# Optimization experiments

Measured on AMD Instinct MI355X. Metric: run time of the kernel, lower is better.

## Reference

```python
import jax, jax.numpy as jnp
import numpy as np

N, E, D, T, R, H = 100000, 800000, 128, 4, 4, 8
DK = D // H
LN_EPS = 1e-5


def _per_type_proj(x, W, b, node_type):
    # x:[N,D], W:[T,D,D], b:[T,D] -> select projection by each node's type
    proj = jnp.einsum('ni,tio->nto', x, W) + b[None]          # [N,T,D]
    return jnp.take_along_axis(proj, node_type[:, None, None], axis=1)[:, 0]  # [N,D]


def setup_inputs() -> dict:
    key = jax.random.key(0)
    ks = jax.random.split(key, 12)
    sW = 1.0 / np.sqrt(D)
    sR = np.sqrt(2.0 / (DK + DK))  # glorot for [dk,dk]
    return {
        'x': jax.random.normal(ks[0], (N, D), jnp.float32),
        'node_type': jax.random.randint(ks[1], (N,), 0, T, jnp.int32),
        'edge_index': jax.random.randint(ks[2], (2, E), 0, N, jnp.int32),
        'edge_type': jax.random.randint(ks[3], (E,), 0, R, jnp.int32),
        'edge_spatial': jnp.zeros((E,), jnp.int32),
        'Wk': jax.random.normal(ks[4], (T, D, D), jnp.float32) * sW,
        'bk': jnp.zeros((T, D), jnp.float32),
        'Wq': jax.random.normal(ks[5], (T, D, D), jnp.float32) * sW,
        'bq': jnp.zeros((T, D), jnp.float32),
        'Wv': jax.random.normal(ks[6], (T, D, D), jnp.float32) * sW,
        'bv': jnp.zeros((T, D), jnp.float32),
        'Wa': jax.random.normal(ks[7], (T, D, D), jnp.float32) * sW,
        'ba': jnp.zeros((T, D), jnp.float32),
        'rel_pri': jnp.ones((R, H), jnp.float32),
        'rel_att': jax.random.normal(ks[8], (R, H, DK, DK), jnp.float32) * sR,
        'rel_msg': jax.random.normal(ks[9], (R, H, DK, DK), jnp.float32) * sR,
        'skip': jnp.ones((T,), jnp.float32),
        'ln_gamma': jnp.ones((T, D), jnp.float32),
        'ln_beta': jnp.zeros((T, D), jnp.float32),
    }


def reference(x, node_type, edge_index, edge_type, edge_spatial,
              Wk, bk, Wq, bq, Wv, bv, Wa, ba,
              rel_pri, rel_att, rel_msg, skip, ln_gamma, ln_beta):
    src, dst = edge_index[0], edge_index[1]  # PyG: row0 = source j, row1 = target i

    # per-type linear projections, selected by node type
    K = _per_type_proj(x, Wk, bk, node_type)
    Q = _per_type_proj(x, Wq, bq, node_type)
    V = _per_type_proj(x, Wv, bv, node_type)

    q_e = Q[dst].reshape(E, H, DK)
    k_e = K[src].reshape(E, H, DK)
    v_e = V[src].reshape(E, H, DK)

    # per-relation transforms without materializing [E,H,DK,DK] gathers
    k_rel = jnp.zeros_like(k_e)
    msg = jnp.zeros_like(v_e)
    for r in range(R):
        m = (edge_type == r)[:, None, None]
        k_rel = k_rel + jnp.where(m, jnp.einsum('ehd,hdk->ehk', k_e, rel_att[r]), 0.0)
        msg = msg + jnp.where(m, jnp.einsum('ehd,hdk->ehk', v_e, rel_msg[r]), 0.0)

    logits = (q_e * k_rel).sum(-1) * rel_pri[edge_type] / np.sqrt(DK)  # [E,H]

    # segment softmax over destination nodes
    seg_max = jax.ops.segment_max(logits, dst, num_segments=N)
    seg_max = jnp.where(jnp.isfinite(seg_max), seg_max, 0.0)
    ex = jnp.exp(logits - seg_max[dst])
    denom = jax.ops.segment_sum(ex, dst, num_segments=N)
    att = ex / denom[dst]  # [E,H]

    aggr = jax.ops.segment_sum(msg * att[:, :, None], dst, num_segments=N)  # [N,H,DK]
    h = jax.nn.gelu(aggr.reshape(N, D), approximate=False)

    trans = _per_type_proj(h, Wa, ba, node_type)
    alpha = jax.nn.sigmoid(skip)[node_type][:, None]
    pre = trans * alpha + x * (1.0 - alpha)

    # per-type LayerNorm
    mu = pre.mean(-1, keepdims=True)
    var = ((pre - mu) ** 2).mean(-1, keepdims=True)
    norm = (pre - mu) * jax.lax.rsqrt(var + LN_EPS)
    return norm * ln_gamma[node_type] + ln_beta[node_type]
```

## Files before the change

kernel.cpp:

```cpp
#include <hip/hip_runtime.h>
#include <math.h>

#define D_DIM 128

using bf16x8 = __attribute__((ext_vector_type(8))) short;
using f32x4  = __attribute__((ext_vector_type(4))) float;

__device__ __forceinline__ unsigned short f2bf(float f) {
    unsigned u = __float_as_uint(f);
    u += 0x7fffu + ((u >> 16) & 1u);
    return (unsigned short)(u >> 16);
}

__global__ __launch_bounds__(256)
void count_types_k(const int* __restrict__ nt, int* __restrict__ blockcnt, int N) {
    __shared__ int wcnt[4][4];
    int tid = threadIdx.x;
    int i = blockIdx.x * 256 + tid;
    int w = tid >> 6, l = tid & 63;
    int t = (i < N) ? nt[i] : -1;
    #pragma unroll
    for (int tt = 0; tt < 4; ++tt) {
        unsigned long long m = __ballot(t == tt);
        if (l == 0) wcnt[w][tt] = __popcll(m);
    }
    __syncthreads();
    if (tid < 4) {
        blockcnt[blockIdx.x * 4 + tid] =
            wcnt[0][tid] + wcnt[1][tid] + wcnt[2][tid] + wcnt[3][tid];
    }
}

__global__ __launch_bounds__(256)
void scan_blocks_k(const int* __restrict__ blockcnt, int nb, int N,
                   int* __restrict__ boff, int* __restrict__ pad_off,
                   int* __restrict__ order_p) {
    __shared__ int tot_s[4];
    __shared__ int po_s[5];
    int tid = threadIdx.x;
    int t = tid >> 6, l = tid & 63;
    int sum = 0;
    for (int base = 0; base < nb; base += 64) {
        int b = base + l;
        sum += (b < nb) ? blockcnt[b * 4 + t] : 0;
    }
    #pragma unroll
    for (int m = 1; m < 64; m <<= 1) sum += __shfl_xor(sum, m);
    if (l == 0) tot_s[t] = sum;
    __syncthreads();
    if (tid == 0) {
        int s = 0;
        for (int tt = 0; tt < 4; ++tt) { po_s[tt] = s; s += ((tot_s[tt] + 63) >> 6) << 6; }
        po_s[4] = s;
        for (int tt = 0; tt < 5; ++tt) pad_off[tt] = po_s[tt];
    }
    __syncthreads();
    #pragma unroll 1
    for (int tt = 0; tt < 4; ++tt) {
        int gs = po_s[tt] + tot_s[tt], ge = po_s[tt + 1];
        for (int i = gs + tid; i < ge; i += 256) order_p[i] = -1;
    }
    for (int i = po_s[4] + tid; i < N + 320; i += 256) order_p[i] = -1;
    __syncthreads();
    int run = po_s[t];
    for (int base = 0; base < nb; base += 64) {
        int b = base + l;
        int v = (b < nb) ? blockcnt[b * 4 + t] : 0;
        int incl = v;
        #pragma unroll
        for (int off = 1; off < 64; off <<= 1) {
            int up = __shfl_up(incl, off);
            if (l >= off) incl += up;
        }
        if (b < nb) boff[b * 4 + t] = run + incl - v;
        run += __shfl(incl, 63);
    }
}

__global__ __launch_bounds__(256)
void scatter_types_k(const int* __restrict__ nt, const int* __restrict__ boff,
                     int* __restrict__ order_p, int N) {
    __shared__ int wbase[4][4];
    int tid = threadIdx.x;
    int i = blockIdx.x * 256 + tid;
    int w = tid >> 6, l = tid & 63;
    int t = (i < N) ? nt[i] : -1;
    int rank = 0;
    #pragma unroll
    for (int tt = 0; tt < 4; ++tt) {
        unsigned long long m = __ballot(t == tt);
        if (l == 0) wbase[w][tt] = __popcll(m);
        if (t == tt) rank = __popcll(m & ((1ull << l) - 1ull));
    }
    __syncthreads();
    if (tid < 4) {
        int run = 0;
        for (int ww = 0; ww < 4; ++ww) { int c = wbase[ww][tid]; wbase[ww][tid] = run; run += c; }
    }
    __syncthreads();
    if (i < N) order_p[boff[blockIdx.x * 4 + t] + wbase[w][t] + rank] = i;
}

__global__ __launch_bounds__(256)
void prep_weights_k(const float* __restrict__ Wk, const float* __restrict__ Wq,
                    const float* __restrict__ Wv, const float* __restrict__ Wa,
                    const float* __restrict__ bk, const float* __restrict__ bv,
                    const float* __restrict__ rel_att, const float* __restrict__ rel_msg,
                    const float* __restrict__ rel_pri,
                    unsigned short* __restrict__ Wqt, unsigned short* __restrict__ Wat,
                    unsigned short* __restrict__ Wkrt, unsigned short* __restrict__ Wvmt,
                    float* __restrict__ bkr, float* __restrict__ bvm) {
    int idx = blockIdx.x * 256 + threadIdx.x;
    int i = idx & 127;
    int col = (idx >> 7) & 127;
    int r = (idx >> 14) & 3;
    int t = idx >> 16;
    int h = col >> 4, k = col & 15;
    {
        const float* wk = Wk + t * 16384 + i * 128 + h * 16;
        const float* wv = Wv + t * 16384 + i * 128 + h * 16;
        const float* ra = rel_att + ((r * 8 + h) * 16) * 16 + k;
        const float* rm = rel_msg + ((r * 8 + h) * 16) * 16 + k;
        float s1 = 0.f, s2 = 0.f;
        #pragma unroll
        for (int d = 0; d < 16; ++d) {
            s1 += wk[d] * ra[d * 16];
            s2 += wv[d] * rm[d * 16];
        }
        Wkrt[idx] = f2bf(s1 * rel_pri[r * 8 + h] * 0.25f);
        Wvmt[idx] = f2bf(s2);
    }
    if (idx < 65536) {
        int t2 = idx >> 14, rem = idx & 16383, row = rem >> 7, col2 = rem & 127;
        int d = (t2 << 14) | (col2 << 7) | row;
        Wqt[d] = f2bf(Wq[idx]);
        Wat[d] = f2bf(Wa[idx]);
    }
    if (idx < 4096) {
        int bi = idx & 2047;
        int col3 = bi & 127, r3 = (bi >> 7) & 3, t3 = bi >> 9;
        int h3 = col3 >> 4, k3 = col3 & 15;
        float s = 0.f;
        if (idx < 2048) {
            #pragma unroll
            for (int d = 0; d < 16; ++d)
                s += bk[t3 * 128 + h3 * 16 + d] * rel_att[((r3 * 8 + h3) * 16 + d) * 16 + k3];
            bkr[bi] = s * rel_pri[r3 * 8 + h3] * 0.25f;
        } else {
            #pragma unroll
            for (int d = 0; d < 16; ++d)
                s += bv[t3 * 128 + h3 * 16 + d] * rel_msg[((r3 * 8 + h3) * 16 + d) * 16 + k3];
            bvm[bi] = s;
        }
    }
}

__global__ void deg_k(const int* __restrict__ ei, int* __restrict__ deg, int E) {
    int e = blockIdx.x * 256 + threadIdx.x;
    if (e < E) atomicAdd(&deg[ei[E + e]], 1);
}
__global__ void scan1_k(const int* __restrict__ deg, int* __restrict__ excl,
                        int* __restrict__ bsum, int N) {
    __shared__ int s[512];
    int i = blockIdx.x * 512 + threadIdx.x;
    int v = (i < N) ? deg[i] : 0;
    s[threadIdx.x] = v;
    __syncthreads();
    for (int off = 1; off < 512; off <<= 1) {
        int t = (threadIdx.x >= off) ? s[threadIdx.x - off] : 0;
        __syncthreads();
        s[threadIdx.x] += t;
        __syncthreads();
    }
    if (i < N) excl[i] = s[threadIdx.x] - v;
    if (threadIdx.x == 511) bsum[blockIdx.x] = s[511];
}
__global__ void scan2_k(int* __restrict__ bsum, int nb) {
    int l = threadIdx.x & 63;
    int run = 0;
    for (int base = 0; base < nb; base += 64) {
        int b = base + l;
        int v = (b < nb) ? bsum[b] : 0;
        int incl = v;
        #pragma unroll
        for (int off = 1; off < 64; off <<= 1) {
            int up = __shfl_up(incl, off);
            if (l >= off) incl += up;
        }
        if (b < nb) bsum[b] = run + incl - v;
        run += __shfl(incl, 63);
    }
}
__global__ void scan3_k(int* __restrict__ excl, const int* __restrict__ bsum, int N) {
    int i = blockIdx.x * 512 + threadIdx.x;
    if (i < N) excl[i] += bsum[blockIdx.x];
}
__global__ void scatter_edges_k(const int* __restrict__ ei, const int* __restrict__ et,
                                const int* __restrict__ off, int* __restrict__ cursor,
                                int* __restrict__ elist, int E) {
    int e = blockIdx.x * 256 + threadIdx.x;
    if (e < E) {
        int dst = ei[E + e];
        int p = off[dst] + atomicAdd(&cursor[dst], 1);
        elist[p] = (ei[e] << 2) | et[e];
    }
}

__global__ __launch_bounds__(256, 4)
void proj_mfma(const float* __restrict__ x, const int* __restrict__ order_p,
               const int* __restrict__ pad_off,
               const unsigned short* __restrict__ Wqt, const float* __restrict__ bq,
               const unsigned short* __restrict__ W_kr_t, const float* __restrict__ bkr,
               const unsigned short* __restrict__ W_vm_t, const float* __restrict__ bvm,
               unsigned short* __restrict__ Qb, unsigned short* __restrict__ KRb,
               unsigned short* __restrict__ VMb, int N) {
    __shared__ unsigned shmem[64 * 128];
    __shared__ int gid_s[64];
    unsigned* xs = shmem;
    char* stageb = (char*)shmem;
    int tid = threadIdx.x;
    int base = blockIdx.x * 64;
    int t = (base >= pad_off[1]) + (base >= pad_off[2]) + (base >= pad_off[3]);

    if (tid < 64) gid_s[tid] = order_p[base + tid];
    __syncthreads();

    {
        int row = tid >> 2, q = tid & 3;
        int g = gid_s[row];
        const float4* xr = (const float4*)(x + (size_t)(g < 0 ? 0 : g) * 128 + q * 32);
        int swz = (row & 7) << 4;
        #pragma unroll
        for (int v4 = 0; v4 < 8; ++v4) {
            float4 f = (g >= 0) ? xr[v4] : make_float4(0.f, 0.f, 0.f, 0.f);
            unsigned ua = (unsigned)f2bf(f.x) | ((unsigned)f2bf(f.y) << 16);
            unsigned ub = (unsigned)f2bf(f.z) | ((unsigned)f2bf(f.w) << 16);
            int c2 = (q * 16 + v4 * 2) * 4;
            xs[(row << 6) + (((c2) ^ swz) >> 2)] = ua;
            xs[(row << 6) + (((c2 + 4) ^ swz) >> 2)] = ub;
        }
    }
    __syncthreads();

    int w = tid >> 6, l = tid & 63;
    int lr = l & 15, lg = l >> 4;

    bf16x8 afr[4][4];
    #pragma unroll
    for (int j = 0; j < 4; ++j) {
        int row = j * 16 + lr;
        #pragma unroll
        for (int ks = 0; ks < 4; ++ks) {
            int byteoff = (ks * 64 + lg * 16) ^ ((lr & 7) << 4);
            afr[j][ks] = *reinterpret_cast<const bf16x8*>(
                reinterpret_cast<const char*>(&xs[row << 6]) + byteoff);
        }
    }
    __syncthreads();

    #pragma unroll 1
    for (int pass = 0; pass < 4; ++pass) {
        int m0 = (pass & 1) * 2;
        const unsigned short* Wp;
        const float* bp;
        unsigned short* dstp;
        if (pass < 2) { Wp = W_kr_t; bp = bkr; dstp = KRb; }
        else          { Wp = W_vm_t; bp = bvm; dstp = VMb; }
        Wp += (size_t)(t * 4 + m0) << 14;
        bp += (t * 4 + m0) * 128;

        #pragma unroll
        for (int ci = 0; ci < 2; ++ci) {
            int c = w * 2 + ci;
            #pragma unroll
            for (int mm = 0; mm < 2; ++mm) {
                const unsigned short* wb = Wp + ((size_t)mm << 14)
                                         + (size_t)(c * 16 + lr) * 128 + lg * 8;
                bf16x8 wfr[4];
                #pragma unroll
                for (int ks = 0; ks < 4; ++ks) wfr[ks] = *(const bf16x8*)(wb + ks * 32);
                f32x4 acc0 = {0.f,0.f,0.f,0.f}, acc1 = {0.f,0.f,0.f,0.f};
                f32x4 acc2 = {0.f,0.f,0.f,0.f}, acc3 = {0.f,0.f,0.f,0.f};
                #pragma unroll
                for (int ks = 0; ks < 4; ++ks) {
                    acc0 = __builtin_amdgcn_mfma_f32_16x16x32_bf16(wfr[ks], afr[0][ks], acc0, 0, 0, 0);
                    acc1 = __builtin_amdgcn_mfma_f32_16x16x32_bf16(wfr[ks], afr[1][ks], acc1, 0, 0, 0);
                    acc2 = __builtin_amdgcn_mfma_f32_16x16x32_bf16(wfr[ks], afr[2][ks], acc2, 0, 0, 0);
                    acc3 = __builtin_amdgcn_mfma_f32_16x16x32_bf16(wfr[ks], afr[3][ks], acc3, 0, 0, 0);
                }
                float4 bb = *(const float4*)&bp[mm * 128 + c * 16 + lg * 4];
                int colb = (mm * 128 + c * 16 + lg * 4) * 2;
                f32x4 accs[4] = {acc0, acc1, acc2, acc3};
                #pragma unroll
                for (int j = 0; j < 4; ++j) {
                    int node = j * 16 + lr;
                    unsigned p0 = (unsigned)f2bf(accs[j][0] + bb.x) | ((unsigned)f2bf(accs[j][1] + bb.y) << 16);
                    unsigned p1 = (unsigned)f2bf(accs[j][2] + bb.z) | ((unsigned)f2bf(accs[j][3] + bb.w) << 16);
                    int byte = (node * 512 + colb) ^ ((node & 7) << 4);
                    *(uint2*)(stageb + byte) = make_uint2(p0, p1);
                }
            }
        }
        __syncthreads();
        #pragma unroll
        for (int i = 0; i < 8; ++i) {
            int row = w * 16 + i * 2 + (l >> 5);
            int l32 = l & 31;
            int byte = (row * 512 + l32 * 16) ^ ((row & 7) << 4);
            uint4 v = *(const uint4*)(stageb + byte);
            int g = gid_s[row];
            if (g >= 0)
                *(uint4*)&dstp[(size_t)g * 512 + (pass & 1) * 256 + l32 * 8] = v;
        }
        __syncthreads();
    }

    #pragma unroll
    for (int ci = 0; ci < 2; ++ci) {
        int c = w * 2 + ci;
        const unsigned short* wb = Wqt + ((size_t)t << 14) + (size_t)(c * 16 + lr) * 128 + lg * 8;
        bf16x8 wfr[4];
        #pragma unroll
        for (int ks = 0; ks < 4; ++ks) wfr[ks] = *(const bf16x8*)(wb + ks * 32);
        f32x4 acc0 = {0.f,0.f,0.f,0.f}, acc1 = {0.f,0.f,0.f,0.f};
        f32x4 acc2 = {0.f,0.f,0.f,0.f}, acc3 = {0.f,0.f,0.f,0.f};
        #pragma unroll
        for (int ks = 0; ks < 4; ++ks) {
            acc0 = __builtin_amdgcn_mfma_f32_16x16x32_bf16(wfr[ks], afr[0][ks], acc0, 0, 0, 0);
            acc1 = __builtin_amdgcn_mfma_f32_16x16x32_bf16(wfr[ks], afr[1][ks], acc1, 0, 0, 0);
            acc2 = __builtin_amdgcn_mfma_f32_16x16x32_bf16(wfr[ks], afr[2][ks], acc2, 0, 0, 0);
            acc3 = __builtin_amdgcn_mfma_f32_16x16x32_bf16(wfr[ks], afr[3][ks], acc3, 0, 0, 0);
        }
        float4 bb = *(const float4*)&bq[t * 128 + c * 16 + lg * 4];
        int colb = (c * 16 + lg * 4) * 2;
        f32x4 accs[4] = {acc0, acc1, acc2, acc3};
        #pragma unroll
        for (int j = 0; j < 4; ++j) {
            int node = j * 16 + lr;
            unsigned p0 = (unsigned)f2bf(accs[j][0] + bb.x) | ((unsigned)f2bf(accs[j][1] + bb.y) << 16);
            unsigned p1 = (unsigned)f2bf(accs[j][2] + bb.z) | ((unsigned)f2bf(accs[j][3] + bb.w) << 16);
            int byte = (node * 256 + colb) ^ ((node & 7) << 4);
            *(uint2*)(stageb + byte) = make_uint2(p0, p1);
        }
    }
    __syncthreads();
    #pragma unroll
    for (int i = 0; i < 4; ++i) {
        int row = w * 16 + i * 4 + (l >> 4);
        int l16 = l & 15;
        int byte = (row * 256 + l16 * 16) ^ ((row & 7) << 4);
        uint4 v = *(const uint4*)(stageb + byte);
        int g = gid_s[row];
        if (g >= 0) *(uint4*)&Qb[(size_t)g * 128 + l16 * 8] = v;
    }
}

__global__ __launch_bounds__(256)
void edge_fused(const unsigned short* __restrict__ Qb,
                const unsigned short* __restrict__ KRb,
                const unsigned short* __restrict__ VMb,
                const int* __restrict__ off, const int* __restrict__ elist,
                float* __restrict__ aggr, int N, int E) {
    int w = threadIdx.x >> 6, l = threadIdx.x & 63;
    int dstA = (blockIdx.x * 4 + w) * 2;
    if (dstA >= N) return;
    int dstB = dstA + 1;
    bool hasB = (dstB < N);
    int q = l >> 4, c = l & 15;

    float QfA[8], QfB[8];
    {
        bf16x8 qv = *(const bf16x8*)&Qb[(size_t)dstA * 128 + c * 8];
        const unsigned* qu = (const unsigned*)&qv;
        #pragma unroll
        for (int i = 0; i < 4; ++i) {
            QfA[2*i]   = __uint_as_float(qu[i] << 16);
            QfA[2*i+1] = __uint_as_float(qu[i] & 0xffff0000u);
        }
    }
    {
        bf16x8 qv = *(const bf16x8*)&Qb[(size_t)(hasB ? dstB : dstA) * 128 + c * 8];
        const unsigned* qu = (const unsigned*)&qv;
        #pragma unroll
        for (int i = 0; i < 4; ++i) {
            QfB[2*i]   = __uint_as_float(qu[i] << 16);
            QfB[2*i+1] = __uint_as_float(qu[i] & 0xffff0000u);
        }
    }

    int eA0 = off[dstA];
    int eA1 = hasB ? off[dstB] : E;
    int eB0 = eA1;
    int eB1 = hasB ? ((dstB == N - 1) ? E : off[dstB + 1]) : eA1;
    int degA = eA1 - eA0;
    int degB = eB1 - eB0;
    int mdeg = max(degA, degB);

    float SA[8] = {0.f,0.f,0.f,0.f,0.f,0.f,0.f,0.f};
    float SB[8] = {0.f,0.f,0.f,0.f,0.f,0.f,0.f,0.f};
    float denA = 0.f, denB = 0.f;

    for (int base = 0; base < mdeg; base += 64) {
        int cntA = min(64, degA - base);
        int cntB = min(64, degB - base);
        int pkA_l = (degA > 0) ? elist[eA0 + min(base + l, degA - 1)] : 0;
        int pkB_l = (degB > 0) ? elist[eB0 + min(base + l, degB - 1)] : 0;
        int mcnt = max(cntA, cntB);
        for (int s = 0; s < mcnt; s += 8) {
            int clA = max(cntA - 1, 0), clB = max(cntB - 1, 0);
            int pkA0 = __shfl(pkA_l, min(s + q, clA));
            int pkA1 = __shfl(pkA_l, min(s + 4 + q, clA));
            int pkB0 = __shfl(pkB_l, min(s + q, clB));
            int pkB1 = __shfl(pkB_l, min(s + 4 + q, clB));
            bf16x8 krA0 = *(const bf16x8*)&KRb[(size_t)pkA0 * 128 + c * 8];
            bf16x8 krA1 = *(const bf16x8*)&KRb[(size_t)pkA1 * 128 + c * 8];
            bf16x8 krB0 = *(const bf16x8*)&KRb[(size_t)pkB0 * 128 + c * 8];
            bf16x8 krB1 = *(const bf16x8*)&KRb[(size_t)pkB1 * 128 + c * 8];
            bf16x8 vmA0 = *(const bf16x8*)&VMb[(size_t)pkA0 * 128 + c * 8];
            bf16x8 vmA1 = *(const bf16x8*)&VMb[(size_t)pkA1 * 128 + c * 8];
            bf16x8 vmB0 = *(const bf16x8*)&VMb[(size_t)pkB0 * 128 + c * 8];
            bf16x8 vmB1 = *(const bf16x8*)&VMb[(size_t)pkB1 * 128 + c * 8];

            const unsigned* ka0 = (const unsigned*)&krA0;
            const unsigned* ka1 = (const unsigned*)&krA1;
            const unsigned* kb0 = (const unsigned*)&krB0;
            const unsigned* kb1 = (const unsigned*)&krB1;
            float dA0 = 0.f, dA1 = 0.f, dB0 = 0.f, dB1 = 0.f;
            #pragma unroll
            for (int i = 0; i < 4; ++i) {
                dA0 = fmaf(QfA[2*i],   __uint_as_float(ka0[i] << 16), dA0);
                dA0 = fmaf(QfA[2*i+1], __uint_as_float(ka0[i] & 0xffff0000u), dA0);
                dA1 = fmaf(QfA[2*i],   __uint_as_float(ka1[i] << 16), dA1);
                dA1 = fmaf(QfA[2*i+1], __uint_as_float(ka1[i] & 0xffff0000u), dA1);
                dB0 = fmaf(QfB[2*i],   __uint_as_float(kb0[i] << 16), dB0);
                dB0 = fmaf(QfB[2*i+1], __uint_as_float(kb0[i] & 0xffff0000u), dB0);
                dB1 = fmaf(QfB[2*i],   __uint_as_float(kb1[i] << 16), dB1);
                dB1 = fmaf(QfB[2*i+1], __uint_as_float(kb1[i] & 0xffff0000u), dB1);
            }
            dA0 += __shfl_xor(dA0, 1);
            dA1 += __shfl_xor(dA1, 1);
            dB0 += __shfl_xor(dB0, 1);
            dB1 += __shfl_xor(dB1, 1);
            float wA0 = (s + q < cntA)     ? __expf(dA0) : 0.f;
            float wA1 = (s + 4 + q < cntA) ? __expf(dA1) : 0.f;
            float wB0 = (s + q < cntB)     ? __expf(dB0) : 0.f;
            float wB1 = (s + 4 + q < cntB) ? __expf(dB1) : 0.f;
            denA += wA0 + wA1;
            denB += wB0 + wB1;

            const unsigned* va0 = (const unsigned*)&vmA0;
            const unsigned* va1 = (const unsigned*)&vmA1;
            const unsigned* vb0 = (const unsigned*)&vmB0;
            const unsigned* vb1 = (const unsigned*)&vmB1;
            #pragma unroll
            for (int i = 0; i < 4; ++i) {
                SA[2*i]   = fmaf(wA0, __uint_as_float(va0[i] << 16), SA[2*i]);
                SA[2*i+1] = fmaf(wA0, __uint_as_float(va0[i] & 0xffff0000u), SA[2*i+1]);
                SA[2*i]   = fmaf(wA1, __uint_as_float(va1[i] << 16), SA[2*i]);
                SA[2*i+1] = fmaf(wA1, __uint_as_float(va1[i] & 0xffff0000u), SA[2*i+1]);
                SB[2*i]   = fmaf(wB0, __uint_as_float(vb0[i] << 16), SB[2*i]);
                SB[2*i+1] = fmaf(wB0, __uint_as_float(vb0[i] & 0xffff0000u), SB[2*i+1]);
                SB[2*i]   = fmaf(wB1, __uint_as_float(vb1[i] << 16), SB[2*i]);
                SB[2*i+1] = fmaf(wB1, __uint_as_float(vb1[i] & 0xffff0000u), SB[2*i+1]);
            }
        }
    }

    #pragma unroll
    for (int m = 16; m <= 32; m <<= 1) {
        denA += __shfl_xor(denA, m);
        denB += __shfl_xor(denB, m);
        #pragma unroll
        for (int i = 0; i < 8; ++i) {
            SA[i] += __shfl_xor(SA[i], m);
            SB[i] += __shfl_xor(SB[i], m);
        }
    }
    float invA = (denA > 0.f) ? 1.f / denA : 0.f;
    float invB = (denB > 0.f) ? 1.f / denB : 0.f;
    float o[8];
    #pragma unroll
    for (int i = 0; i < 8; ++i) o[i] = (q == 1) ? SB[i] * invB : SA[i] * invA;
    int sd = (q == 1) ? dstB : dstA;
    if (q == 0 || (q == 1 && hasB)) {
        *(float4*)&aggr[(size_t)sd * 128 + c * 8]     = make_float4(o[0], o[1], o[2], o[3]);
        *(float4*)&aggr[(size_t)sd * 128 + c * 8 + 4] = make_float4(o[4], o[5], o[6], o[7]);
    }
}

__global__ __launch_bounds__(256)
void node_out_mfma(const float* __restrict__ aggr, const float* __restrict__ x,
                   const int* __restrict__ order_p, const int* __restrict__ pad_off,
                   const unsigned short* __restrict__ Wat, const float* __restrict__ ba,
                   const float* __restrict__ skip, const float* __restrict__ gamma,
                   const float* __restrict__ beta, float* __restrict__ out, int N) {
    __shared__ unsigned hsm[64 * 64];
    __shared__ int gid_s[64];
    int tid = threadIdx.x;
    int base = blockIdx.x * 64;
    int t = (base >= pad_off[1]) + (base >= pad_off[2]) + (base >= pad_off[3]);

    if (tid < 64) gid_s[tid] = order_p[base + tid];
    __syncthreads();

    {
        int row = tid >> 2, q = tid & 3;
        int g = gid_s[row];
        const float4* ar = (const float4*)(aggr + (size_t)(g < 0 ? 0 : g) * 128 + q * 32);
        int swz = (row & 7) << 4;
        #pragma unroll
        for (int v4 = 0; v4 < 8; ++v4) {
            float4 f = (g >= 0) ? ar[v4] : make_float4(0.f, 0.f, 0.f, 0.f);
            float g0 = 0.5f * f.x * (1.f + erff(f.x * 0.70710678118654752f));
            float g1 = 0.5f * f.y * (1.f + erff(f.y * 0.70710678118654752f));
            float g2 = 0.5f * f.z * (1.f + erff(f.z * 0.70710678118654752f));
            float g3 = 0.5f * f.w * (1.f + erff(f.w * 0.70710678118654752f));
            unsigned ua = (unsigned)f2bf(g0) | ((unsigned)f2bf(g1) << 16);
            unsigned ub = (unsigned)f2bf(g2) | ((unsigned)f2bf(g3) << 16);
            int c2 = (q * 16 + v4 * 2) * 4;
            hsm[(row << 6) + (((c2) ^ swz) >> 2)] = ua;
            hsm[(row << 6) + (((c2 + 4) ^ swz) >> 2)] = ub;
        }
    }
    __syncthreads();

    int w = tid >> 6, l = tid & 63;
    int rowbase = w * 16, lr = l & 15, lg = l >> 4;
    int myrow = rowbase + lr;

    bf16x8 afr[4];
    #pragma unroll
    for (int ks = 0; ks < 4; ++ks) {
        int byteoff = (ks * 64 + lg * 16) ^ ((lr & 7) << 4);
        afr[ks] = *reinterpret_cast<const bf16x8*>(
            reinterpret_cast<const char*>(&hsm[myrow << 6]) + byteoff);
    }

    float al = 1.f / (1.f + __expf(-skip[t]));
    int g = gid_s[myrow];

    float pre[8][4];
    float s = 0.f, sq = 0.f;

    #pragma unroll
    for (int c = 0; c < 8; ++c) {
        const unsigned short* wb = Wat + ((size_t)t << 14) + (size_t)(c * 16 + lr) * 128 + lg * 8;
        f32x4 acc = {0.f, 0.f, 0.f, 0.f};
        #pragma unroll
        for (int ks = 0; ks < 4; ++ks)
            acc = __builtin_amdgcn_mfma_f32_16x16x32_bf16(
                *(const bf16x8*)(wb + ks * 32), afr[ks], acc, 0, 0, 0);
        float4 bav = *(const float4*)&ba[t * 128 + c * 16 + lg * 4];
        float4 xv = (g >= 0) ? *(const float4*)&x[(size_t)g * 128 + c * 16 + lg * 4]
                             : make_float4(0.f, 0.f, 0.f, 0.f);
        float p0 = (acc[0] + bav.x) * al + xv.x * (1.f - al);
        float p1 = (acc[1] + bav.y) * al + xv.y * (1.f - al);
        float p2 = (acc[2] + bav.z) * al + xv.z * (1.f - al);
        float p3 = (acc[3] + bav.w) * al + xv.w * (1.f - al);
        pre[c][0] = p0; pre[c][1] = p1; pre[c][2] = p2; pre[c][3] = p3;
        s += p0 + p1 + p2 + p3;
        sq += p0 * p0 + p1 * p1 + p2 * p2 + p3 * p3;
    }

    s  += __shfl_xor(s, 16);  sq += __shfl_xor(sq, 16);
    s  += __shfl_xor(s, 32);  sq += __shfl_xor(sq, 32);
    float mu = s * (1.f / 128.f);
    float var = sq * (1.f / 128.f) - mu * mu;
    float rs = rsqrtf(fmaxf(var, 0.f) + 1e-5f);

    #pragma unroll
    for (int c = 0; c < 8; ++c) {
        float4 ga = *(const float4*)&gamma[t * 128 + c * 16 + lg * 4];
        float4 be = *(const float4*)&beta[t * 128 + c * 16 + lg * 4];
        float4 o;
        o.x = (pre[c][0] - mu) * rs * ga.x + be.x;
        o.y = (pre[c][1] - mu) * rs * ga.y + be.y;
        o.z = (pre[c][2] - mu) * rs * ga.z + be.z;
        o.w = (pre[c][3] - mu) * rs * ga.w + be.w;
        if (g >= 0) *(float4*)&out[(size_t)g * 128 + c * 16 + lg * 4] = o;
    }
}

extern "C" void kernel_launch(void* const* d_in, const int* in_sizes, int n_in,
                              void* d_out, int out_size, void* d_ws, size_t ws_size,
                              hipStream_t stream) {
    const float* x   = (const float*)d_in[0];
    const int*   nt  = (const int*)d_in[1];
    const int*   ei  = (const int*)d_in[2];
    const int*   et  = (const int*)d_in[3];
    const float* Wk = (const float*)d_in[5];  const float* bk = (const float*)d_in[6];
    const float* Wq = (const float*)d_in[7];  const float* bq = (const float*)d_in[8];
    const float* Wv = (const float*)d_in[9];  const float* bv = (const float*)d_in[10];
    const float* Wa = (const float*)d_in[11]; const float* ba = (const float*)d_in[12];
    const float* rel_pri = (const float*)d_in[13];
    const float* rel_att = (const float*)d_in[14];
    const float* rel_msg = (const float*)d_in[15];
    const float* skip    = (const float*)d_in[16];
    const float* gamma   = (const float*)d_in[17];
    const float* beta    = (const float*)d_in[18];

    const int N = in_sizes[0] / 128;
    const int E = in_sizes[3];
    const int NB = (N + 511) / 512;
    const int NB256 = (N + 255) / 256;

    unsigned short* Qb  = (unsigned short*)d_ws;
    unsigned short* KRb = Qb + (size_t)N * 128;
    unsigned short* VMb = KRb + (size_t)N * 512;
    unsigned short* Wqt = VMb + (size_t)N * 512;
    unsigned short* Wat = Wqt + 65536;
    unsigned short* Wkrt = Wat + 65536;
    unsigned short* Wvmt = Wkrt + 262144;
    float* bkr = (float*)(Wvmt + 262144);
    float* bvm = bkr + 2048;
    int* order_p = (int*)(bvm + 2048);
    int* blockcnt = order_p + N + 320;
    int* boff     = blockcnt + NB256 * 4;
    int* pad_off  = boff + NB256 * 4;
    int* deg     = pad_off + 8;
    int* cursorD = deg + N;
    int* off     = cursorD + N;
    int* bsum    = off + N;
    int* elist   = bsum + NB + 8;
    float* aggr  = (float*)d_out;

    hipMemsetAsync(deg, 0, (size_t)(2 * N) * sizeof(int), stream);

    count_types_k<<<NB256, 256, 0, stream>>>(nt, blockcnt, N);
    scan_blocks_k<<<1, 256, 0, stream>>>(blockcnt, NB256, N, boff, pad_off, order_p);
    scatter_types_k<<<NB256, 256, 0, stream>>>(nt, boff, order_p, N);

    prep_weights_k<<<1024, 256, 0, stream>>>(Wk, Wq, Wv, Wa, bk, bv, rel_att, rel_msg,
                                             rel_pri, Wqt, Wat, Wkrt, Wvmt, bkr, bvm);

    deg_k<<<(E + 255) / 256, 256, 0, stream>>>(ei, deg, E);
    scan1_k<<<NB, 512, 0, stream>>>(deg, off, bsum, N);
    scan2_k<<<1, 64, 0, stream>>>(bsum, NB);
    scan3_k<<<NB, 512, 0, stream>>>(off, bsum, N);
    scatter_edges_k<<<(E + 255) / 256, 256, 0, stream>>>(ei, et, off, cursorD, elist, E);

    int nb64 = (N + 252 + 63) / 64;
    proj_mfma<<<nb64, 256, 0, stream>>>(x, order_p, pad_off, Wqt, bq, Wkrt, bkr, Wvmt, bvm,
                                        Qb, KRb, VMb, N);
    int npairs = (N + 1) / 2;
    edge_fused<<<(npairs + 3) / 4, 256, 0, stream>>>(Qb, KRb, VMb, off, elist, aggr, N, E);
    node_out_mfma<<<nb64, 256, 0, stream>>>(aggr, x, order_p, pad_off, Wat, ba, skip,
                                            gamma, beta, (float*)d_out, N);
}
```

Baseline: 392.3 us.

## Interleave per-relation K and V projections and fuse scan passes

Stores the relation-transformed K and V rows for each node and relation contiguously in one buffer, so the edge kernel's gathers for a (source, relation) pair hit one 512-byte span instead of two separate arrays. This aims to improve locality of the random gathers in the edge kernel. It also merges the single-block scan of block sums and the offset-add kernel into one kernel where each block sums its preceding block totals itself. That removes a launch and a serial step, at the cost of redundant prefix sums across blocks.

```diff
diff --git a/kernel.cpp b/kernel.cpp
--- a/kernel.cpp
+++ b/kernel.cpp
@@ -175,25 +175,20 @@
     if (i < N) excl[i] = s[threadIdx.x] - v;
     if (threadIdx.x == 511) bsum[blockIdx.x] = s[511];
 }
-__global__ void scan2_k(int* __restrict__ bsum, int nb) {
-    int l = threadIdx.x & 63;
-    int run = 0;
-    for (int base = 0; base < nb; base += 64) {
-        int b = base + l;
-        int v = (b < nb) ? bsum[b] : 0;
-        int incl = v;
-        #pragma unroll
-        for (int off = 1; off < 64; off <<= 1) {
-            int up = __shfl_up(incl, off);
-            if (l >= off) incl += up;
-        }
-        if (b < nb) bsum[b] = run + incl - v;
-        run += __shfl(incl, 63);
-    }
-}
-__global__ void scan3_k(int* __restrict__ excl, const int* __restrict__ bsum, int N) {
-    int i = blockIdx.x * 512 + threadIdx.x;
-    if (i < N) excl[i] += bsum[blockIdx.x];
+__global__ void scan23_k(int* __restrict__ excl, const int* __restrict__ bsum, int N) {
+    __shared__ int pre_s;
+    int b = blockIdx.x;
+    int tid = threadIdx.x, l = tid & 63;
+    if (tid < 64) {
+        int sum = 0;
+        for (int j = l; j < b; j += 64) sum += bsum[j];
+        #pragma unroll
+        for (int m = 1; m < 64; m <<= 1) sum += __shfl_xor(sum, m);
+        if (l == 0) pre_s = sum;
+    }
+    __syncthreads();
+    int i = b * 512 + tid;
+    if (i < N) excl[i] += pre_s;
 }
 __global__ void scatter_edges_k(const int* __restrict__ ei, const int* __restrict__ et,
                                 const int* __restrict__ off, int* __restrict__ cursor,
@@ -212,8 +207,7 @@
                const unsigned short* __restrict__ Wqt, const float* __restrict__ bq,
                const unsigned short* __restrict__ W_kr_t, const float* __restrict__ bkr,
                const unsigned short* __restrict__ W_vm_t, const float* __restrict__ bvm,
-               unsigned short* __restrict__ Qb, unsigned short* __restrict__ KRb,
-               unsigned short* __restrict__ VMb, int N) {
+               unsigned short* __restrict__ Qb, unsigned short* __restrict__ KVb, int N) {
     __shared__ unsigned shmem[64 * 128];
     __shared__ int gid_s[64];
     unsigned* xs = shmem;
@@ -260,14 +254,10 @@
 
     #pragma unroll 1
     for (int pass = 0; pass < 4; ++pass) {
+        bool isKR = (pass < 2);
         int m0 = (pass & 1) * 2;
-        const unsigned short* Wp;
-        const float* bp;
-        unsigned short* dstp;
-        if (pass < 2) { Wp = W_kr_t; bp = bkr; dstp = KRb; }
-        else          { Wp = W_vm_t; bp = bvm; dstp = VMb; }
-        Wp += (size_t)(t * 4 + m0) << 14;
-        bp += (t * 4 + m0) * 128;
+        const unsigned short* Wp = (isKR ? W_kr_t : W_vm_t) + ((size_t)(t * 4 + m0) << 14);
+        const float* bp = (isKR ? bkr : bvm) + (t * 4 + m0) * 128;
 
         #pragma unroll
         for (int ci = 0; ci < 2; ++ci) {
@@ -309,8 +299,11 @@
             int byte = (row * 512 + l32 * 16) ^ ((row & 7) << 4);
             uint4 v = *(const uint4*)(stageb + byte);
             int g = gid_s[row];
-            if (g >= 0)
-                *(uint4*)&dstp[(size_t)g * 512 + (pass & 1) * 256 + l32 * 8] = v;
+            if (g >= 0) {
+                int mat = m0 + (l32 >> 4);
+                int coloff = (l32 & 15) * 8 + (isKR ? 0 : 128);
+                *(uint4*)&KVb[((size_t)g * 4 + mat) * 256 + coloff] = v;
+            }
         }
         __syncthreads();
     }
@@ -357,8 +350,7 @@
 
 __global__ __launch_bounds__(256)
 void edge_fused(const unsigned short* __restrict__ Qb,
-                const unsigned short* __restrict__ KRb,
-                const unsigned short* __restrict__ VMb,
+                const unsigned short* __restrict__ KVb,
                 const int* __restrict__ off, const int* __restrict__ elist,
                 float* __restrict__ aggr, int N, int E) {
     int w = threadIdx.x >> 6, l = threadIdx.x & 63;
@@ -412,14 +404,14 @@
             int pkA1 = __shfl(pkA_l, min(s + 4 + q, clA));
             int pkB0 = __shfl(pkB_l, min(s + q, clB));
             int pkB1 = __shfl(pkB_l, min(s + 4 + q, clB));
-            bf16x8 krA0 = *(const bf16x8*)&KRb[(size_t)pkA0 * 128 + c * 8];
-            bf16x8 krA1 = *(const bf16x8*)&KRb[(size_t)pkA1 * 128 + c * 8];
-            bf16x8 krB0 = *(const bf16x8*)&KRb[(size_t)pkB0 * 128 + c * 8];
-            bf16x8 krB1 = *(const bf16x8*)&KRb[(size_t)pkB1 * 128 + c * 8];
-            bf16x8 vmA0 = *(const bf16x8*)&VMb[(size_t)pkA0 * 128 + c * 8];
-            bf16x8 vmA1 = *(const bf16x8*)&VMb[(size_t)pkA1 * 128 + c * 8];
-            bf16x8 vmB0 = *(const bf16x8*)&VMb[(size_t)pkB0 * 128 + c * 8];
-            bf16x8 vmB1 = *(const bf16x8*)&VMb[(size_t)pkB1 * 128 + c * 8];
+            bf16x8 krA0 = *(const bf16x8*)&KVb[(size_t)pkA0 * 256 + c * 8];
+            bf16x8 krA1 = *(const bf16x8*)&KVb[(size_t)pkA1 * 256 + c * 8];
+            bf16x8 krB0 = *(const bf16x8*)&KVb[(size_t)pkB0 * 256 + c * 8];
+            bf16x8 krB1 = *(const bf16x8*)&KVb[(size_t)pkB1 * 256 + c * 8];
+            bf16x8 vmA0 = *(const bf16x8*)&KVb[(size_t)pkA0 * 256 + 128 + c * 8];
+            bf16x8 vmA1 = *(const bf16x8*)&KVb[(size_t)pkA1 * 256 + 128 + c * 8];
+            bf16x8 vmB0 = *(const bf16x8*)&KVb[(size_t)pkB0 * 256 + 128 + c * 8];
+            bf16x8 vmB1 = *(const bf16x8*)&KVb[(size_t)pkB1 * 256 + 128 + c * 8];
 
             const unsigned* ka0 = (const unsigned*)&krA0;
             const unsigned* ka1 = (const unsigned*)&krA1;
@@ -605,9 +597,8 @@
     const int NB256 = (N + 255) / 256;
 
     unsigned short* Qb  = (unsigned short*)d_ws;
-    unsigned short* KRb = Qb + (size_t)N * 128;
-    unsigned short* VMb = KRb + (size_t)N * 512;
-    unsigned short* Wqt = VMb + (size_t)N * 512;
+    unsigned short* KVb = Qb + (size_t)N * 128;
+    unsigned short* Wqt = KVb + (size_t)N * 1024;
     unsigned short* Wat = Wqt + 65536;
     unsigned short* Wkrt = Wat + 65536;
     unsigned short* Wvmt = Wkrt + 262144;
@@ -635,15 +626,14 @@
 
     deg_k<<<(E + 255) / 256, 256, 0, stream>>>(ei, deg, E);
     scan1_k<<<NB, 512, 0, stream>>>(deg, off, bsum, N);
-    scan2_k<<<1, 64, 0, stream>>>(bsum, NB);
-    scan3_k<<<NB, 512, 0, stream>>>(off, bsum, N);
+    scan23_k<<<NB, 512, 0, stream>>>(off, bsum, N);
     scatter_edges_k<<<(E + 255) / 256, 256, 0, stream>>>(ei, et, off, cursorD, elist, E);
 
     int nb64 = (N + 252 + 63) / 64;
     proj_mfma<<<nb64, 256, 0, stream>>>(x, order_p, pad_off, Wqt, bq, Wkrt, bkr, Wvmt, bvm,
-                                        Qb, KRb, VMb, N);
+                                        Qb, KVb, N);
     int npairs = (N + 1) / 2;
-    edge_fused<<<(npairs + 3) / 4, 256, 0, stream>>>(Qb, KRb, VMb, off, elist, aggr, N, E);
+    edge_fused<<<(npairs + 3) / 4, 256, 0, stream>>>(Qb, KVb, off, elist, aggr, N, E);
     node_out_mfma<<<nb64, 256, 0, stream>>>(aggr, x, order_p, pad_off, Wat, ba, skip,
                                             gamma, beta, (float*)d_out, N);
 }
```

Measured after the change: 392.3 us. Within noise of the previous version (+0.0%).
